# Optimization experiments

Measured on AMD Instinct MI355X. Metric: run time of the kernel, lower is better.

Reference implementation:

```python
import jax, jax.numpy as jnp
import numpy as np

NUM_SAMPLES = 10000  # hardcoded in the torch module
BATCH, K = 512, 16


def setup_inputs() -> dict:
    key = jax.random.key(0)
    k1, k2 = jax.random.split(key)
    mean = jax.random.normal(k1, (BATCH, K), dtype=jnp.float32)
    var = jax.random.uniform(k2, (BATCH, K), dtype=jnp.float32)  # variances must be >= 0
    return {"mean": mean, "var": var}


def reference(mean, var):
    # z ~ N(0,1), shape (*, K, S); fixed key => deterministic MC draw
    z = jax.random.normal(jax.random.key(42), (*mean.shape, NUM_SAMPLES), dtype=mean.dtype)
    # affine transform to N(mean, var) samples
    sample = z * jnp.sqrt(var)[..., None] + mean[..., None]
    # softmax over the category axis K (dim=-2), per MC sample
    softmax_out = jax.nn.softmax(sample, axis=-2)
    out_mean = jnp.mean(softmax_out, axis=-1)
    # torch.var defaults to unbiased (correction=1)
    out_var = jnp.var(softmax_out, axis=-1, ddof=1)
    return out_mean, out_var
```

## Files before the change

kernel.cpp:

```cpp
#include <hip/hip_runtime.h>
#include <cstdint>
#include <math.h>


typedef float f32x2 __attribute__((ext_vector_type(2)));

#define NSAMP 10000
#define HALF_N 40960000u
#define THREADS 256
#define WAVES 4

#define LOG2E 1.44269504088896340736f
#define NLN2 -0.69314718055994530942f
#define SQRT_LN2 0.83255461115769775635f

__device__ __forceinline__ uint32_t rotl32(uint32_t x, int r) {
    return (x << r) | (x >> (32 - r));
}

__device__ __forceinline__ void tf2x32(uint32_t x0, uint32_t x1,
                                       uint32_t& o0, uint32_t& o1) {
    const uint32_t ks1 = 42u;
    const uint32_t ks2 = 0x1BD11BDAu ^ 42u;
    x1 += ks1;
#define TF_R(r) { x0 += x1; x1 = rotl32(x1, r); x1 ^= x0; }
    TF_R(13) TF_R(15) TF_R(26) TF_R(6)   x0 += ks1; x1 += ks2 + 1u;
    TF_R(17) TF_R(29) TF_R(16) TF_R(24)  x0 += ks2; x1 += 2u;
    TF_R(13) TF_R(15) TF_R(26) TF_R(6)                x1 += ks1 + 3u;
    TF_R(17) TF_R(29) TF_R(16) TF_R(24)  x0 += ks1; x1 += ks2 + 4u;
    TF_R(13) TF_R(15) TF_R(26) TF_R(6)   x0 += ks2; x1 += 5u;
#undef TF_R
    o0 = x0;
    o1 = x1;
}

__device__ __forceinline__ f32x2 u2_from_bits(uint32_t ba, uint32_t bb) {
    f32x2 f;
    f.x = __uint_as_float((ba >> 9) | 0x3F800000u);
    f.y = __uint_as_float((bb >> 9) | 0x3F800000u);
    f = f - (f32x2){1.0f, 1.0f};
    return __builtin_elementwise_fma(f, (f32x2){2.0f, 2.0f},
                                     (f32x2){-0.99999994f, -0.99999994f});
}

__device__ __forceinline__ f32x2 erfinv2(f32x2 x) {
    f32x2 t = __builtin_elementwise_fma(-x, x, (f32x2){1.0f, 1.0f});
    f32x2 l;
    l.x = __builtin_amdgcn_logf(t.x);
    l.y = __builtin_amdgcn_logf(t.y);
    f32x2 wm = __builtin_elementwise_fma((f32x2){NLN2, NLN2}, l,
                                         (f32x2){-2.5f, -2.5f});
#define P9(P, W, C) P = __builtin_elementwise_fma(P, W, (f32x2){C, C});
    f32x2 p1 = {2.81022636e-08f, 2.81022636e-08f};
    P9(p1, wm, 3.43273939e-07f)
    P9(p1, wm, -3.5233877e-06f)
    P9(p1, wm, -4.39150654e-06f)
    P9(p1, wm, 0.00021858087f)
    P9(p1, wm, -0.00125372503f)
    P9(p1, wm, -0.00417768164f)
    P9(p1, wm, 0.246640727f)
    P9(p1, wm, 1.50140941f)
    f32x2 sq;
    sq.x = __builtin_amdgcn_sqrtf(-l.x);
    sq.y = __builtin_amdgcn_sqrtf(-l.y);
    f32x2 wt = __builtin_elementwise_fma((f32x2){SQRT_LN2, SQRT_LN2}, sq,
                                         (f32x2){-3.0f, -3.0f});
    f32x2 p2 = {-0.000200214257f, -0.000200214257f};
    P9(p2, wt, 0.000100950558f)
    P9(p2, wt, 0.00134934322f)
    P9(p2, wt, -0.00367342844f)
    P9(p2, wt, 0.00573950773f)
    P9(p2, wt, -0.0076224613f)
    P9(p2, wt, 0.00943887047f)
    P9(p2, wt, 1.00167406f)
    P9(p2, wt, 2.83297682f)
#undef P9
    f32x2 p;
    p.x = (l.x > -7.2134752f) ? p1.x : p2.x;
    p.y = (l.y > -7.2134752f) ? p1.y : p2.y;
    return p * x;
}

__device__ __forceinline__ float qsum4(float v) {
    v += __shfl_xor(v, 1);
    v += __shfl_xor(v, 2);
    return v;
}
__device__ __forceinline__ float xsum16(float v) {
    v += __shfl_xor(v, 4);
    v += __shfl_xor(v, 8);
    v += __shfl_xor(v, 16);
    v += __shfl_xor(v, 32);
    return v;
}

__device__ __forceinline__ void sg_accumulate(const float* __restrict__ mean,
                                              const float* __restrict__ var,
                                              int b, int s_begin, int s_end,
                                              float (*s_mu)[16], float (*s_sv)[16],
                                              float* s_red, float* s_fin) {
    const int tid = threadIdx.x;

    if (tid < 32) {
        int h = tid >> 4, k = tid & 15;
        int bg = b + 256 * h;
        s_mu[h][k] = LOG2E * mean[bg * 16 + k];
        s_sv[h][k] = (LOG2E * 1.41421356237309515f) * sqrtf(var[bg * 16 + k]);
    }
    __syncthreads();

    const int a4 = (tid & 3) * 4;
    const int sgrp = tid >> 2;

    f32x2 mu0[2], sv0[2], mu1[2], sv1[2];
#pragma unroll
    for (int p = 0; p < 2; p++) {
        mu0[p] = *(const f32x2*)&s_mu[0][a4 + 2 * p];
        sv0[p] = *(const f32x2*)&s_sv[0][a4 + 2 * p];
        mu1[p] = *(const f32x2*)&s_mu[1][a4 + 2 * p];
        sv1[p] = *(const f32x2*)&s_sv[1][a4 + 2 * p];
    }

    f32x2 as0[2], aq0[2], as1[2], aq1[2];
#pragma unroll
    for (int p = 0; p < 2; p++) {
        as0[p] = (f32x2){0.f, 0.f}; aq0[p] = (f32x2){0.f, 0.f};
        as1[p] = (f32x2){0.f, 0.f}; aq1[p] = (f32x2){0.f, 0.f};
    }

    const uint32_t base = (uint32_t)((b * 16 + a4) * 10000);

    for (int s = s_begin + sgrp; s < s_end; s += 64) {
        f32x2 e0[2], e1[2];
#pragma unroll
        for (int p = 0; p < 2; p++) {
            uint32_t ia = base + (uint32_t)(p * 20000) + (uint32_t)s;
            uint32_t ib = ia + 10000u;
            uint32_t a0, a1, b0, b1;
            tf2x32(ia, ia + HALF_N, a0, a1);
            tf2x32(ib, ib + HALF_N, b0, b1);
            f32x2 z0 = erfinv2(u2_from_bits(a0, b0));
            f32x2 z1 = erfinv2(u2_from_bits(a1, b1));
            e0[p] = __builtin_elementwise_fma(z0, sv0[p], mu0[p]);
            e1[p] = __builtin_elementwise_fma(z1, sv1[p], mu1[p]);
        }
#pragma unroll
        for (int p = 0; p < 2; p++) {
            e0[p].x = __builtin_amdgcn_exp2f(e0[p].x);
            e0[p].y = __builtin_amdgcn_exp2f(e0[p].y);
            e1[p].x = __builtin_amdgcn_exp2f(e1[p].x);
            e1[p].y = __builtin_amdgcn_exp2f(e1[p].y);
        }
        f32x2 q0 = e0[0] + e0[1];
        f32x2 q1 = e1[0] + e1[1];
        float r0 = qsum4(q0.x + q0.y);
        float r1 = qsum4(q1.x + q1.y);
        float inv0 = __builtin_amdgcn_rcpf(r0);
        float inv1 = __builtin_amdgcn_rcpf(r1);
        f32x2 iv0 = {inv0, inv0}, iv1 = {inv1, inv1};
#pragma unroll
        for (int p = 0; p < 2; p++) {
            f32x2 p0 = e0[p] * iv0;
            f32x2 p1 = e1[p] * iv1;
            as0[p] += p0; aq0[p] = __builtin_elementwise_fma(p0, p0, aq0[p]);
            as1[p] += p1; aq1[p] = __builtin_elementwise_fma(p1, p1, aq1[p]);
        }
    }

    const int lane = tid & 63, wave = tid >> 6;
    float vals[16] = { as0[0].x, aq0[0].x, as1[0].x, aq1[0].x,
                       as0[0].y, aq0[0].y, as1[0].y, aq1[0].y,
                       as0[1].x, aq0[1].x, as1[1].x, aq1[1].x,
                       as0[1].y, aq0[1].y, as1[1].y, aq1[1].y };
#pragma unroll
    for (int i = 0; i < 16; i++) {
        float r = xsum16(vals[i]);
        if (lane < 4) {
            int k = lane * 4 + (i >> 2);
            s_red[wave * 64 + k * 4 + (i & 3)] = r;
        }
    }
    __syncthreads();

    if (tid < 64) {
        float t = 0.f;
#pragma unroll
        for (int w = 0; w < WAVES; w++) t += s_red[w * 64 + tid];
        s_fin[tid] = t;
    }
    __syncthreads();
}

template <int NCH>
__global__ __launch_bounds__(THREADS, 4)
void sg_partial(const float* __restrict__ mean, const float* __restrict__ var,
                float* __restrict__ ws) {
    __shared__ __attribute__((aligned(8))) float s_mu[2][16];
    __shared__ __attribute__((aligned(8))) float s_sv[2][16];
    __shared__ float s_red[WAVES * 64], s_fin[64];
    const int b = blockIdx.x / NCH;
    const int chunk = blockIdx.x % NCH;
    const int c0 = chunk * (NSAMP / NCH);
    sg_accumulate(mean, var, b, c0, c0 + NSAMP / NCH, s_mu, s_sv, s_red, s_fin);
    if (threadIdx.x < 64) ws[blockIdx.x * 64 + threadIdx.x] = s_fin[threadIdx.x];
}

__global__ __launch_bounds__(256)
void sg_finalize(const float* __restrict__ ws, float* __restrict__ out, int nch) {
    int t = blockIdx.x * blockDim.x + threadIdx.x;
    if (t >= 8192) return;
    int k = t & 15, h = (t >> 4) & 1, b = t >> 5;
    float sum = 0.f, sq = 0.f;
    for (int c = 0; c < nch; c++) {
        const float* p = ws + ((b * nch + c) * 64 + k * 4 + 2 * h);
        sum += p[0];
        sq += p[1];
    }
    float mu = sum * (1.0f / 10000.0f);
    float vr = (sq - sum * mu) * (1.0f / 9999.0f);
    int bg = b + 256 * h;
    out[bg * 16 + k] = mu;
    out[8192 + bg * 16 + k] = vr;
}

__global__ __launch_bounds__(THREADS, 4)
void sg_kernel(const float* __restrict__ mean, const float* __restrict__ var,
               float* __restrict__ out) {
    __shared__ __attribute__((aligned(8))) float s_mu[2][16];
    __shared__ __attribute__((aligned(8))) float s_sv[2][16];
    __shared__ float s_red[WAVES * 64], s_fin[64];
    const int b = blockIdx.x;
    sg_accumulate(mean, var, b, 0, NSAMP, s_mu, s_sv, s_red, s_fin);
    const int tid = threadIdx.x;
    if (tid < 32) {
        int h = tid >> 4, k = tid & 15;
        float sum = s_fin[k * 4 + 2 * h + 0];
        float sq  = s_fin[k * 4 + 2 * h + 1];
        float mu = sum * (1.0f / 10000.0f);
        float vr = (sq - sum * mu) * (1.0f / 9999.0f);
        int bg = b + 256 * h;
        out[bg * 16 + k] = mu;
        out[8192 + bg * 16 + k] = vr;
    }
}

extern "C" void kernel_launch(void* const* d_in, const int* in_sizes, int n_in,
                              void* d_out, int out_size, void* d_ws, size_t ws_size,
                              hipStream_t stream) {
    const float* mean = (const float*)d_in[0];
    const float* var  = (const float*)d_in[1];
    float* out = (float*)d_out;
    float* ws = (float*)d_ws;
    if (ws_size >= 256 * 8 * 64 * sizeof(float)) {
        sg_partial<8><<<256 * 8, THREADS, 0, stream>>>(mean, var, ws);
        sg_finalize<<<32, 256, 0, stream>>>(ws, out, 8);
    } else if (ws_size >= 256 * 4 * 64 * sizeof(float)) {
        sg_partial<4><<<256 * 4, THREADS, 0, stream>>>(mean, var, ws);
        sg_finalize<<<32, 256, 0, stream>>>(ws, out, 4);
    } else {
        sg_kernel<<<256, THREADS, 0, stream>>>(mean, var, out);
    }
}
```

Baseline: 157.3 us.

## Skip erfinv tail branch wave-uniformly, double block size, unroll sample loop by two

Evaluates the erfinv tail polynomial and sqrt only when some lane in the wave needs it, using __any, so the common central-region case skips that work. It also raises the block to 512 threads (8 waves), drops the 8-chunk split in favour of 4 chunks, unrolls the sample loop by two, packs the two quad reductions into one vector shuffle sequence, and uses the rotate builtin. Tail samples are rare, so the wave-uniform branch should usually be skipped, but the larger blocks and fewer chunks change occupancy and how work is spread across CUs. The 8-wave reduction and 512-wide tiling must still line up with the launch.

New measurement: 158.3 us. No clear change (+0.6%).

```diff
diff --git a/kernel.cpp b/kernel.cpp
--- a/kernel.cpp
+++ b/kernel.cpp
@@ -7,15 +7,17 @@
 
 #define NSAMP 10000
 #define HALF_N 40960000u
-#define THREADS 256
-#define WAVES 4
+#define THREADS 512
+#define WAVES 8
+#define SGROUPS (THREADS / 4)
 
 #define LOG2E 1.44269504088896340736f
 #define NLN2 -0.69314718055994530942f
 #define SQRT_LN2 0.83255461115769775635f
+#define TAIL_TH -7.2134752f
 
 __device__ __forceinline__ uint32_t rotl32(uint32_t x, int r) {
-    return (x << r) | (x >> (32 - r));
+    return __builtin_rotateleft32(x, (unsigned)r);
 }
 
 __device__ __forceinline__ void tf2x32(uint32_t x0, uint32_t x1,
@@ -60,31 +62,34 @@
     P9(p1, wm, -0.00417768164f)
     P9(p1, wm, 0.246640727f)
     P9(p1, wm, 1.50140941f)
-    f32x2 sq;
-    sq.x = __builtin_amdgcn_sqrtf(-l.x);
-    sq.y = __builtin_amdgcn_sqrtf(-l.y);
-    f32x2 wt = __builtin_elementwise_fma((f32x2){SQRT_LN2, SQRT_LN2}, sq,
-                                         (f32x2){-3.0f, -3.0f});
-    f32x2 p2 = {-0.000200214257f, -0.000200214257f};
-    P9(p2, wt, 0.000100950558f)
-    P9(p2, wt, 0.00134934322f)
-    P9(p2, wt, -0.00367342844f)
-    P9(p2, wt, 0.00573950773f)
-    P9(p2, wt, -0.0076224613f)
-    P9(p2, wt, 0.00943887047f)
-    P9(p2, wt, 1.00167406f)
-    P9(p2, wt, 2.83297682f)
+    f32x2 p = p1;
+    if (__any((l.x < TAIL_TH) || (l.y < TAIL_TH))) {
+        f32x2 sq;
+        sq.x = __builtin_amdgcn_sqrtf(-l.x);
+        sq.y = __builtin_amdgcn_sqrtf(-l.y);
+        f32x2 wt = __builtin_elementwise_fma((f32x2){SQRT_LN2, SQRT_LN2}, sq,
+                                             (f32x2){-3.0f, -3.0f});
+        f32x2 p2 = {-0.000200214257f, -0.000200214257f};
+        P9(p2, wt, 0.000100950558f)
+        P9(p2, wt, 0.00134934322f)
+        P9(p2, wt, -0.00367342844f)
+        P9(p2, wt, 0.00573950773f)
+        P9(p2, wt, -0.0076224613f)
+        P9(p2, wt, 0.00943887047f)
+        P9(p2, wt, 1.00167406f)
+        P9(p2, wt, 2.83297682f)
+        p.x = (l.x > TAIL_TH) ? p1.x : p2.x;
+        p.y = (l.y > TAIL_TH) ? p1.y : p2.y;
+    }
 #undef P9
-    f32x2 p;
-    p.x = (l.x > -7.2134752f) ? p1.x : p2.x;
-    p.y = (l.y > -7.2134752f) ? p1.y : p2.y;
     return p * x;
 }
 
-__device__ __forceinline__ float qsum4(float v) {
-    v += __shfl_xor(v, 1);
-    v += __shfl_xor(v, 2);
-    return v;
+__device__ __forceinline__ f32x2 qsum4_pk(f32x2 v) {
+    f32x2 r = v;
+    r.x += __shfl_xor(r.x, 1); r.y += __shfl_xor(r.y, 1);
+    r.x += __shfl_xor(r.x, 2); r.y += __shfl_xor(r.y, 2);
+    return r;
 }
 __device__ __forceinline__ float xsum16(float v) {
     v += __shfl_xor(v, 4);
@@ -94,6 +99,49 @@
     return v;
 }
 
+struct SgState {
+    f32x2 mu0[2], sv0[2], mu1[2], sv1[2];
+    f32x2 as0[2], aq0[2], as1[2], aq1[2];
+    uint32_t base;
+};
+
+__device__ __forceinline__ void sg_sample(SgState& st, int s) {
+    f32x2 e0[2], e1[2];
+#pragma unroll
+    for (int p = 0; p < 2; p++) {
+        uint32_t ia = st.base + (uint32_t)(p * 20000) + (uint32_t)s;
+        uint32_t ib = ia + 10000u;
+        uint32_t a0, a1, b0, b1;
+        tf2x32(ia, ia + HALF_N, a0, a1);
+        tf2x32(ib, ib + HALF_N, b0, b1);
+        f32x2 z0 = erfinv2(u2_from_bits(a0, b0));
+        f32x2 z1 = erfinv2(u2_from_bits(a1, b1));
+        e0[p] = __builtin_elementwise_fma(z0, st.sv0[p], st.mu0[p]);
+        e1[p] = __builtin_elementwise_fma(z1, st.sv1[p], st.mu1[p]);
+    }
+#pragma unroll
+    for (int p = 0; p < 2; p++) {
+        e0[p].x = __builtin_amdgcn_exp2f(e0[p].x);
+        e0[p].y = __builtin_amdgcn_exp2f(e0[p].y);
+        e1[p].x = __builtin_amdgcn_exp2f(e1[p].x);
+        e1[p].y = __builtin_amdgcn_exp2f(e1[p].y);
+    }
+    f32x2 q0 = e0[0] + e0[1];
+    f32x2 q1 = e1[0] + e1[1];
+    f32x2 rr = {q0.x + q0.y, q1.x + q1.y};
+    rr = qsum4_pk(rr);
+    f32x2 iv0 = {0.f, 0.f}, iv1 = {0.f, 0.f};
+    iv0.x = iv0.y = __builtin_amdgcn_rcpf(rr.x);
+    iv1.x = iv1.y = __builtin_amdgcn_rcpf(rr.y);
+#pragma unroll
+    for (int p = 0; p < 2; p++) {
+        f32x2 p0 = e0[p] * iv0;
+        f32x2 p1 = e1[p] * iv1;
+        st.as0[p] += p0; st.aq0[p] = __builtin_elementwise_fma(p0, p0, st.aq0[p]);
+        st.as1[p] += p1; st.aq1[p] = __builtin_elementwise_fma(p1, p1, st.aq1[p]);
+    }
+}
+
 __device__ __forceinline__ void sg_accumulate(const float* __restrict__ mean,
                                               const float* __restrict__ var,
                                               int b, int s_begin, int s_end,
@@ -112,66 +160,30 @@
     const int a4 = (tid & 3) * 4;
     const int sgrp = tid >> 2;
 
-    f32x2 mu0[2], sv0[2], mu1[2], sv1[2];
-#pragma unroll
-    for (int p = 0; p < 2; p++) {
-        mu0[p] = *(const f32x2*)&s_mu[0][a4 + 2 * p];
-        sv0[p] = *(const f32x2*)&s_sv[0][a4 + 2 * p];
-        mu1[p] = *(const f32x2*)&s_mu[1][a4 + 2 * p];
-        sv1[p] = *(const f32x2*)&s_sv[1][a4 + 2 * p];
-    }
-
-    f32x2 as0[2], aq0[2], as1[2], aq1[2];
-#pragma unroll
-    for (int p = 0; p < 2; p++) {
-        as0[p] = (f32x2){0.f, 0.f}; aq0[p] = (f32x2){0.f, 0.f};
-        as1[p] = (f32x2){0.f, 0.f}; aq1[p] = (f32x2){0.f, 0.f};
-    }
-
-    const uint32_t base = (uint32_t)((b * 16 + a4) * 10000);
-
-    for (int s = s_begin + sgrp; s < s_end; s += 64) {
-        f32x2 e0[2], e1[2];
-#pragma unroll
-        for (int p = 0; p < 2; p++) {
-            uint32_t ia = base + (uint32_t)(p * 20000) + (uint32_t)s;
-            uint32_t ib = ia + 10000u;
-            uint32_t a0, a1, b0, b1;
-            tf2x32(ia, ia + HALF_N, a0, a1);
-            tf2x32(ib, ib + HALF_N, b0, b1);
-            f32x2 z0 = erfinv2(u2_from_bits(a0, b0));
-            f32x2 z1 = erfinv2(u2_from_bits(a1, b1));
-            e0[p] = __builtin_elementwise_fma(z0, sv0[p], mu0[p]);
-            e1[p] = __builtin_elementwise_fma(z1, sv1[p], mu1[p]);
-        }
-#pragma unroll
-        for (int p = 0; p < 2; p++) {
-            e0[p].x = __builtin_amdgcn_exp2f(e0[p].x);
-            e0[p].y = __builtin_amdgcn_exp2f(e0[p].y);
-            e1[p].x = __builtin_amdgcn_exp2f(e1[p].x);
-            e1[p].y = __builtin_amdgcn_exp2f(e1[p].y);
-        }
-        f32x2 q0 = e0[0] + e0[1];
-        f32x2 q1 = e1[0] + e1[1];
-        float r0 = qsum4(q0.x + q0.y);
-        float r1 = qsum4(q1.x + q1.y);
-        float inv0 = __builtin_amdgcn_rcpf(r0);
-        float inv1 = __builtin_amdgcn_rcpf(r1);
-        f32x2 iv0 = {inv0, inv0}, iv1 = {inv1, inv1};
-#pragma unroll
-        for (int p = 0; p < 2; p++) {
-            f32x2 p0 = e0[p] * iv0;
-            f32x2 p1 = e1[p] * iv1;
-            as0[p] += p0; aq0[p] = __builtin_elementwise_fma(p0, p0, aq0[p]);
-            as1[p] += p1; aq1[p] = __builtin_elementwise_fma(p1, p1, aq1[p]);
-        }
-    }
+    SgState st;
+#pragma unroll
+    for (int p = 0; p < 2; p++) {
+        st.mu0[p] = *(const f32x2*)&s_mu[0][a4 + 2 * p];
+        st.sv0[p] = *(const f32x2*)&s_sv[0][a4 + 2 * p];
+        st.mu1[p] = *(const f32x2*)&s_mu[1][a4 + 2 * p];
+        st.sv1[p] = *(const f32x2*)&s_sv[1][a4 + 2 * p];
+        st.as0[p] = (f32x2){0.f, 0.f}; st.aq0[p] = (f32x2){0.f, 0.f};
+        st.as1[p] = (f32x2){0.f, 0.f}; st.aq1[p] = (f32x2){0.f, 0.f};
+    }
+    st.base = (uint32_t)((b * 16 + a4) * 10000);
+
+    int s = s_begin + sgrp;
+    for (; s + SGROUPS < s_end; s += 2 * SGROUPS) {
+        sg_sample(st, s);
+        sg_sample(st, s + SGROUPS);
+    }
+    for (; s < s_end; s += SGROUPS) sg_sample(st, s);
 
     const int lane = tid & 63, wave = tid >> 6;
-    float vals[16] = { as0[0].x, aq0[0].x, as1[0].x, aq1[0].x,
-                       as0[0].y, aq0[0].y, as1[0].y, aq1[0].y,
-                       as0[1].x, aq0[1].x, as1[1].x, aq1[1].x,
-                       as0[1].y, aq0[1].y, as1[1].y, aq1[1].y };
+    float vals[16] = { st.as0[0].x, st.aq0[0].x, st.as1[0].x, st.aq1[0].x,
+                       st.as0[0].y, st.aq0[0].y, st.as1[0].y, st.aq1[0].y,
+                       st.as0[1].x, st.aq0[1].x, st.as1[1].x, st.aq1[1].x,
+                       st.as0[1].y, st.aq0[1].y, st.as1[1].y, st.aq1[1].y };
 #pragma unroll
     for (int i = 0; i < 16; i++) {
         float r = xsum16(vals[i]);
@@ -192,7 +204,7 @@
 }
 
 template <int NCH>
-__global__ __launch_bounds__(THREADS, 4)
+__global__ __launch_bounds__(THREADS, 8)
 void sg_partial(const float* __restrict__ mean, const float* __restrict__ var,
                 float* __restrict__ ws) {
     __shared__ __attribute__((aligned(8))) float s_mu[2][16];
@@ -223,7 +235,7 @@
     out[8192 + bg * 16 + k] = vr;
 }
 
-__global__ __launch_bounds__(THREADS, 4)
+__global__ __launch_bounds__(THREADS, 8)
 void sg_kernel(const float* __restrict__ mean, const float* __restrict__ var,
                float* __restrict__ out) {
     __shared__ __attribute__((aligned(8))) float s_mu[2][16];
@@ -251,10 +263,7 @@
     const float* var  = (const float*)d_in[1];
     float* out = (float*)d_out;
     float* ws = (float*)d_ws;
-    if (ws_size >= 256 * 8 * 64 * sizeof(float)) {
-        sg_partial<8><<<256 * 8, THREADS, 0, stream>>>(mean, var, ws);
-        sg_finalize<<<32, 256, 0, stream>>>(ws, out, 8);
-    } else if (ws_size >= 256 * 4 * 64 * sizeof(float)) {
+    if (ws_size >= 256 * 4 * 64 * sizeof(float)) {
         sg_partial<4><<<256 * 4, THREADS, 0, stream>>>(mean, var, ws);
         sg_finalize<<<32, 256, 0, stream>>>(ws, out, 4);
     } else {
```
